# Performance work log

Measured on AMD Instinct MI355X. Metric: run time of the kernel, lower is better.

The kernel has to match this reference:

```python
import jax, jax.numpy as jnp
import numpy as np

HIDDEN = 1024
HEADS = 16
MEM = 2
D_H = HIDDEN // HEADS
NEG = -1.0e9


def setup_inputs() -> dict:
    key = jax.random.key(0)
    ks = jax.random.split(key, 8)
    B, M, N = 16, 512, 512
    s = 1.0 / np.sqrt(HIDDEN)
    return {
        "x": jax.random.normal(ks[0], (B, M, HIDDEN), dtype=jnp.float32),
        "y": jax.random.normal(ks[1], (B, N, HIDDEN), dtype=jnp.float32),
        "mask_x": jax.random.randint(ks[2], (B, M), 0, 2, dtype=jnp.int64),
        "mask_y": jax.random.randint(ks[3], (B, N), 0, 2, dtype=jnp.int64),
        "Wx": jax.random.normal(ks[4], (HIDDEN, HIDDEN), dtype=jnp.float32) * s,
        "Wy": jax.random.normal(ks[5], (HIDDEN, HIDDEN), dtype=jnp.float32) * s,
        "x_memory": jax.random.normal(ks[6], (MEM, HIDDEN), dtype=jnp.float32),
        "y_memory": jax.random.normal(ks[7], (MEM, HIDDEN), dtype=jnp.float32),
    }


def _project(t, mem, W):
    # prepend memory tokens, then linear (torch Linear: t @ W^T), split heads
    B = t.shape[0]
    t_mem = jnp.concatenate([jnp.broadcast_to(mem[None], (B, MEM, HIDDEN)), t], axis=1)
    proj = t_mem @ W.T
    proj = proj.reshape(B, t_mem.shape[1], HEADS, D_H)
    return t_mem, proj


def reference(x, y, mask_x, mask_y, Wx, Wy, x_memory, y_memory):
    B = x.shape[0]
    mem_mask = jnp.ones((B, MEM), dtype=mask_x.dtype)
    mx = jnp.concatenate([mem_mask, mask_x], axis=1)  # [B, M+MEM]
    my = jnp.concatenate([mem_mask, mask_y], axis=1)  # [B, N+MEM]

    X_mem, X_proj = _project(x, x_memory, Wx)  # [B,Mm,H], [B,Mm,heads,d_h]
    Y_mem, Y_proj = _project(y, y_memory, Wy)

    # affinity: [B, heads, Mm, Nm]
    aff = jnp.einsum("bmhd,bnhd->bhmn", X_proj, Y_proj)
    aff = jnp.where(mx[:, None, :, None] == 0, NEG, aff)
    aff = jnp.where(my[:, None, None, :] == 0, NEG, aff)

    attn_X = jnp.mean(jax.nn.softmax(aff, axis=2), axis=1)  # [B, Mm, Nm]
    attn_Y = jnp.mean(jax.nn.softmax(aff, axis=3), axis=1)  # [B, Mm, Nm]

    X_in_Y = jnp.einsum("bmn,bmh->bnh", attn_X, X_mem)[:, MEM:, :]  # [B, N, H]
    Y_in_X = jnp.einsum("bmn,bnh->bmh", attn_Y, Y_mem)[:, MEM:, :]  # [B, M, H]
    return X_in_Y, Y_in_X
```

## Files before the change

### kernel.cpp

```cpp
#include <hip/hip_runtime.h>

#define B_   16
#define SEQ  512
#define MM   514
#define HID  1024
#define NH   16
#define DH   64
#define KP   544
#define MTOT (B_ * MM)
#define UNI  (1.0f/514.0f)

typedef unsigned short us;
typedef __attribute__((ext_vector_type(4))) float f32x4;
typedef __attribute__((ext_vector_type(8))) short short8;
typedef __attribute__((ext_vector_type(8))) _Float16 half8;

__device__ __forceinline__ us f2bf(float f) {
  unsigned int u = __float_as_uint(f);
  u = (u + 0x7FFFu + ((u >> 16) & 1u)) >> 16;
  return (us)u;
}
__device__ __forceinline__ float bf2f(us h) {
  return __uint_as_float(((unsigned int)h) << 16);
}
__device__ __forceinline__ us f2h(float f) {
  _Float16 h = (_Float16)f;
  return *(us*)&h;
}
__device__ __forceinline__ unsigned cvt_pk_bf16(float lo, float hi) {
  unsigned d;
  asm("v_cvt_pk_bf16_f32 %0, %1, %2" : "=v"(d) : "v"(lo), "v"(hi));
  return d;
}

__global__ __launch_bounds__(256) void prepack(
    const float* __restrict__ x, const float* __restrict__ y,
    const float* __restrict__ xm, const float* __restrict__ ym,
    const float* __restrict__ Wx, const float* __restrict__ Wy,
    us* __restrict__ Abf, us* __restrict__ Wbf) {
  const int tid = threadIdx.x;
  const int row = blockIdx.x * 4 + (tid >> 6);
  const int path = blockIdx.y;
  const int lane = tid & 63;
  const float* src;
  us* dst;
  if (row < MTOT) {
    const int gb = row / MM, gt = row - gb * MM;
    const float* tin = path ? y : x;
    const float* mv  = path ? ym : xm;
    src = (gt < 2) ? (mv + (size_t)gt * HID)
                   : (tin + ((size_t)(gb * SEQ + gt - 2)) * HID);
    dst = Abf + ((size_t)(path * MTOT + row)) * HID;
  } else {
    const int o = row - MTOT;
    src = (path ? Wy : Wx) + (size_t)o * HID;
    dst = Wbf + ((size_t)(path * HID + o)) * HID;
  }
  const float* s = src + lane * 16;
  f32x4 v0 = *(const f32x4*)(s);
  f32x4 v1 = *(const f32x4*)(s + 4);
  f32x4 v2 = *(const f32x4*)(s + 8);
  f32x4 v3 = *(const f32x4*)(s + 12);
  uint4 w0, w1;
  w0.x = cvt_pk_bf16(v0[0], v0[1]);  w0.y = cvt_pk_bf16(v0[2], v0[3]);
  w0.z = cvt_pk_bf16(v1[0], v1[1]);  w0.w = cvt_pk_bf16(v1[2], v1[3]);
  w1.x = cvt_pk_bf16(v2[0], v2[1]);  w1.y = cvt_pk_bf16(v2[2], v2[3]);
  w1.z = cvt_pk_bf16(v3[0], v3[1]);  w1.w = cvt_pk_bf16(v3[2], v3[3]);
  *(uint4*)(dst + lane * 16)     = w0;
  *(uint4*)(dst + lane * 16 + 8) = w1;
}

__global__ __launch_bounds__(256) void proj_fused2(
    const us* __restrict__ Abf, const us* __restrict__ Wbf,
    us* __restrict__ Px, us* __restrict__ Py) {
  const int lin = blockIdx.x + 8 * (blockIdx.y + 65 * blockIdx.z);
  const int work = (lin & 7) * 130 + (lin >> 3);
  const int path = (work >= 520) ? 1 : 0;
  const int wrem = work - path * 520;
  const int mt = wrem >> 3, nt = wrem & 7;
  us* P = path ? Py : Px;
  const us* Ab = Abf + (size_t)path * MTOT * HID;
  const us* Wb = Wbf + (size_t)path * HID * HID;

  __shared__ __align__(16) us As[128 * 40];
  __shared__ __align__(16) us Bs[128 * 40];
  const int tid = threadIdx.x;
  const int lane = tid & 63, wave = tid >> 6;
  const int c = lane & 15, q = lane >> 4;
  const int wr = wave >> 1, wc = wave & 1;

  const int srow = tid >> 1, sch = (tid & 1) * 16;
  const int grow = mt * 128 + srow;
  const us* asrc = (grow < MTOT) ? (Ab + (size_t)grow * HID + sch) : nullptr;
  const us* bsrc = Wb + (size_t)(nt * 128 + srow) * HID + sch;
  us* wAp = &As[srow * 40 + sch];
  us* wBp = &Bs[srow * 40 + sch];
  const us* rA = &As[(wr * 64 + c) * 40 + q * 8];
  const us* rB = &Bs[(wc * 64 + c) * 40 + q * 8];

  f32x4 acc[4][4];
#pragma unroll
  for (int i = 0; i < 4; i++)
#pragma unroll
    for (int j = 0; j < 4; j++) acc[i][j] = (f32x4){0.f, 0.f, 0.f, 0.f};

  uint4 z4 = {0u, 0u, 0u, 0u};
  uint4 pa0 = z4, pa1 = z4, pb0, pb1;
  if (asrc) { pa0 = *(const uint4*)asrc; pa1 = *(const uint4*)(asrc + 8); }
  pb0 = *(const uint4*)bsrc; pb1 = *(const uint4*)(bsrc + 8);

  for (int kk = 0; kk < HID; kk += 32) {
    __syncthreads();
    *(uint4*)wAp       = pa0;
    *(uint4*)(wAp + 8) = pa1;
    *(uint4*)wBp       = pb0;
    *(uint4*)(wBp + 8) = pb1;
    __syncthreads();
    if (kk + 32 < HID) {
      if (asrc) {
        pa0 = *(const uint4*)(asrc + kk + 32);
        pa1 = *(const uint4*)(asrc + kk + 32 + 8);
      }
      pb0 = *(const uint4*)(bsrc + kk + 32);
      pb1 = *(const uint4*)(bsrc + kk + 32 + 8);
    }
    short8 a[4], bb[4];
#pragma unroll
    for (int i = 0; i < 4; i++) a[i] = *(const short8*)(rA + i * 16 * 40);
#pragma unroll
    for (int j = 0; j < 4; j++) bb[j] = *(const short8*)(rB + j * 16 * 40);
#pragma unroll
    for (int i = 0; i < 4; i++)
#pragma unroll
      for (int j = 0; j < 4; j++)
        acc[i][j] = __builtin_amdgcn_mfma_f32_16x16x32_bf16(a[i], bb[j], acc[i][j], 0, 0, 0);
  }
#pragma unroll
  for (int i = 0; i < 4; i++) {
#pragma unroll
    for (int r = 0; r < 4; r++) {
      int gr = mt * 128 + wr * 64 + i * 16 + q * 4 + r;
      if (gr < MTOT) {
        size_t rb = (size_t)gr * HID;
#pragma unroll
        for (int j = 0; j < 4; j++)
          P[rb + nt * 128 + wc * 64 + j * 16 + c] = f2bf(acc[i][j][r]);
      }
    }
  }
}

__device__ __forceinline__ void stage_bf(
    us* Xs, const us* P, int b, int r0, int h, int tid) {
#pragma unroll
  for (int i = 0; i < 2; i++) {
    int idx = tid + i * 256;
    int row = idx >> 3, qq = idx & 7;
    *(uint4*)&Xs[row * 72 + qq * 8] =
        *(const uint4*)(P + ((size_t)(b * MM + min(r0 + row, MM - 1))) * HID + h * DH + qq * 8);
  }
}

__global__ __launch_bounds__(512) void sums_v4(
    const us* __restrict__ Px, const us* __restrict__ Py,
    const int* __restrict__ mx, const int* __restrict__ my,
    float* __restrict__ Sums) {
  const int lin = blockIdx.x;
  const int work = (lin & 7) * 160 + (lin >> 3);
  const int b = work / 80;
  const int rem = work - b * 80;
  const int h = rem / 5;
  const int nc = rem - h * 5;
  const int n0 = nc * 128;
  __shared__ __align__(16) us Ys[128 * 72];
  __shared__ __align__(16) us Xs[2][64 * 72];
  __shared__ float cS2[4][128];
  __shared__ float rS2[2][576];
  __shared__ int myS[128];
  __shared__ int mxS[576];
  const int tid = threadIdx.x;
  const int lane = tid & 63, wave = tid >> 6;
  const int c = lane & 15, q = lane >> 4;
  const int strip = wave & 3, cgrp = wave >> 2;
  const int row8 = tid >> 3, qq = tid & 7;

  for (int i = tid; i < 128; i += 512) {
    int n = n0 + i;
    myS[i] = (n >= MM) ? 0 : ((n < 2) ? 1 : my[b * SEQ + n - 2]);
  }
  for (int i = tid; i < 576; i += 512)
    mxS[i] = (i >= MM) ? 0 : ((i < 2) ? 1 : mx[b * SEQ + i - 2]);
  {
#pragma unroll
    for (int it = 0; it < 2; it++) {
      int idx = tid + it * 512;
      int row = idx >> 3, q8 = idx & 7;
      int grow = min(n0 + row, MM - 1);
      *(uint4*)&Ys[row * 72 + q8 * 8] =
          *(const uint4*)(Py + ((size_t)(b * MM + grow)) * HID + h * DH + q8 * 8);
    }
  }
  {
    int grow = min(row8, MM - 1);
    *(uint4*)&Xs[0][row8 * 72 + qq * 8] =
        *(const uint4*)(Px + ((size_t)(b * MM + grow)) * HID + h * DH + qq * 8);
  }
  __syncthreads();

  const size_t base = ((size_t)(b * NH + h)) * MM;
  const size_t COLOFF = (size_t)B_ * NH * MM;

  int myReg[4];
#pragma unroll
  for (int ss = 0; ss < 4; ss++) myReg[ss] = myS[cgrp * 64 + ss * 16 + c];

  float colAcc[4] = {0.f, 0.f, 0.f, 0.f};

  for (int mt = 0; mt < 9; mt++) {
    const us* xb = &Xs[mt & 1][0];
    uint4 nx = {0u, 0u, 0u, 0u};
    if (mt + 1 < 9) {
      int grow = min((mt + 1) * 64 + row8, MM - 1);
      nx = *(const uint4*)(Px + ((size_t)(b * MM + grow)) * HID + h * DH + qq * 8);
    }
    short8 a0 = *(const short8*)&xb[(strip * 16 + c) * 72 + q * 8];
    short8 a1 = *(const short8*)&xb[(strip * 16 + c) * 72 + q * 8 + 32];
    int rm[4];
#pragma unroll
    for (int r = 0; r < 4; r++) rm[r] = mxS[mt * 64 + strip * 16 + q * 4 + r];
    float rowp[4] = {0.f, 0.f, 0.f, 0.f};
#pragma unroll
    for (int ss = 0; ss < 4; ss++) {
      int nloc = cgrp * 64 + ss * 16 + c;
      short8 b0 = *(const short8*)&Ys[nloc * 72 + q * 8];
      short8 b1 = *(const short8*)&Ys[nloc * 72 + q * 8 + 32];
      f32x4 av = (f32x4){0.f, 0.f, 0.f, 0.f};
      av = __builtin_amdgcn_mfma_f32_16x16x32_bf16(a0, b0, av, 0, 0, 0);
      av = __builtin_amdgcn_mfma_f32_16x16x32_bf16(a1, b1, av, 0, 0, 0);
#pragma unroll
      for (int r = 0; r < 4; r++) {
        float e = (rm[r] && myReg[ss]) ? __expf(av[r]) : 0.f;
        rowp[r] += e;
        colAcc[ss] += e;
      }
    }
#pragma unroll
    for (int d = 1; d < 16; d <<= 1)
#pragma unroll
      for (int r = 0; r < 4; r++) rowp[r] += __shfl_xor(rowp[r], d, 16);
    if (c == 0) {
#pragma unroll
      for (int r = 0; r < 4; r++)
        rS2[cgrp][mt * 64 + strip * 16 + q * 4 + r] = rowp[r];
    }
    if (mt + 1 < 9)
      *(uint4*)&Xs[(mt + 1) & 1][row8 * 72 + qq * 8] = nx;
    __syncthreads();
  }

#pragma unroll
  for (int ss = 0; ss < 4; ss++) {
    colAcc[ss] += __shfl_xor(colAcc[ss], 16);
    colAcc[ss] += __shfl_xor(colAcc[ss], 32);
  }
  if (q == 0) {
#pragma unroll
    for (int ss = 0; ss < 4; ss++)
      cS2[strip][cgrp * 64 + ss * 16 + c] = colAcc[ss];
  }
  __syncthreads();
  for (int i = tid; i < 128; i += 512) {
    int n = n0 + i;
    if (n < MM)
      Sums[COLOFF + base + n] = cS2[0][i] + cS2[1][i] + cS2[2][i] + cS2[3][i];
  }
  for (int i = tid; i < 576; i += 512) {
    if (i < MM) atomicAdd(&Sums[base + i], rS2[0][i] + rS2[1][i]);
  }
}

__global__ __launch_bounds__(256) void inv_kernel(float* __restrict__ Sums) {
  int i = blockIdx.x * 256 + threadIdx.x;
  if (i < 2 * B_ * NH * MM) {
    float s = Sums[i];
    Sums[i] = (s > 0.f) ? (1.f / s) : -1.f;
  }
}

__global__ __launch_bounds__(256) void attn_swz(
    const us* __restrict__ Px, const us* __restrict__ Py,
    const int* __restrict__ mx, const int* __restrict__ my,
    const float* __restrict__ Inv,
    us* __restrict__ attnXT, us* __restrict__ attnY) {
  const int lin = blockIdx.x;
  const int work = (lin & 7) * 162 + (lin >> 3);
  const int b = work / 81;
  const int rem = work - b * 81;
  const int mt = rem / 9;
  const int nt = rem - mt * 9;
  __shared__ __align__(16) us Xs[64 * 72];
  __shared__ __align__(16) us Ys[64 * 72];
  const int tid = threadIdx.x;
  const int lane = tid & 63, wave = tid >> 6;
  const int c = lane & 15, q = lane >> 4;
  const size_t COLOFF = (size_t)B_ * NH * MM;

  int mreg[4], rm[4], ncol[4], cm[4];
#pragma unroll
  for (int r = 0; r < 4; r++) {
    mreg[r] = mt * 64 + wave * 16 + q * 4 + r;
    rm[r] = (mreg[r] >= MM) ? 0 : ((mreg[r] < 2) ? 1 : mx[b * SEQ + mreg[r] - 2]);
  }
#pragma unroll
  for (int s = 0; s < 4; s++) {
    ncol[s] = nt * 64 + s * 16 + c;
    cm[s] = (ncol[s] >= MM) ? 0 : ((ncol[s] < 2) ? 1 : my[b * SEQ + ncol[s] - 2]);
  }

  float aX[4][4], aY[4][4];
#pragma unroll
  for (int s = 0; s < 4; s++)
#pragma unroll
    for (int r = 0; r < 4; r++) { aX[s][r] = 0.f; aY[s][r] = 0.f; }

  for (int h = 0; h < NH; h++) {
    __syncthreads();
    stage_bf(Xs, Px, b, mt * 64, h, tid);
    stage_bf(Ys, Py, b, nt * 64, h, tid);
    __syncthreads();
    short8 a0 = *(const short8*)&Xs[(wave * 16 + c) * 72 + q * 8];
    short8 a1 = *(const short8*)&Xs[(wave * 16 + c) * 72 + q * 8 + 32];
    const size_t base = ((size_t)(b * NH + h)) * MM;
    float invR[4];
#pragma unroll
    for (int r = 0; r < 4; r++) invR[r] = Inv[base + min(mreg[r], MM - 1)];
#pragma unroll
    for (int s = 0; s < 4; s++) {
      float invC = Inv[COLOFF + base + min(ncol[s], MM - 1)];
      short8 b0 = *(const short8*)&Ys[(s * 16 + c) * 72 + q * 8];
      short8 b1 = *(const short8*)&Ys[(s * 16 + c) * 72 + q * 8 + 32];
      f32x4 av = (f32x4){0.f, 0.f, 0.f, 0.f};
      av = __builtin_amdgcn_mfma_f32_16x16x32_bf16(a0, b0, av, 0, 0, 0);
      av = __builtin_amdgcn_mfma_f32_16x16x32_bf16(a1, b1, av, 0, 0, 0);
#pragma unroll
      for (int r = 0; r < 4; r++) {
        float e = (rm[r] && cm[s]) ? __expf(av[r]) : 0.f;
        aY[s][r] += (invR[r] < 0.f) ? UNI : e * invR[r];
        aX[s][r] += (invC < 0.f) ? UNI : e * invC;
      }
    }
  }
#pragma unroll
  for (int s = 0; s < 4; s++) {
    if (ncol[s] < MM) {
      us* xrow = attnXT + ((size_t)(b * MM + ncol[s])) * KP;
      if (mreg[3] < MM) {
        uint2 w;
        w.x = (unsigned)f2h(aX[s][0] * 0.0625f) | ((unsigned)f2h(aX[s][1] * 0.0625f) << 16);
        w.y = (unsigned)f2h(aX[s][2] * 0.0625f) | ((unsigned)f2h(aX[s][3] * 0.0625f) << 16);
        *(uint2*)&xrow[mreg[0]] = w;
      } else {
#pragma unroll
        for (int r = 0; r < 4; r++)
          if (mreg[r] < MM) xrow[mreg[r]] = f2h(aX[s][r] * 0.0625f);
      }
#pragma unroll
      for (int r = 0; r < 4; r++)
        if (mreg[r] < MM)
          attnY[((size_t)(b * MM + mreg[r])) * KP + ncol[s]] = f2h(aY[s][r] * 0.0625f);
    }
  }
}

__global__ __launch_bounds__(256) void transpose_fused(
    const float* __restrict__ x, const float* __restrict__ y,
    const float* __restrict__ xm, const float* __restrict__ ym,
    us* __restrict__ XTx, us* __restrict__ XTy) {
  const int kt = blockIdx.x, ot = blockIdx.y;
  const int b = blockIdx.z & 15, path = blockIdx.z >> 4;
  const float* tin  = path ? y  : x;
  const float* mvec = path ? ym : xm;
  us* XT            = path ? XTy : XTx;
  __shared__ __align__(16) us T[64 * 40];
  const int tid = threadIdx.x;
  {
    const int row = tid >> 3;
    const int col8 = (tid & 7) * 8;
    const int kg = kt * 32 + row;
    const float* src = (kg < 2) ? (mvec + (size_t)kg * HID + ot * 64 + col8)
                     : (kg < MM) ? (tin + ((size_t)(b * SEQ + kg - 2)) * HID + ot * 64 + col8)
                                 : nullptr;
    f32x4 v0 = (f32x4){0.f, 0.f, 0.f, 0.f};
    f32x4 v1 = (f32x4){0.f, 0.f, 0.f, 0.f};
    if (src) { v0 = *(const f32x4*)src; v1 = *(const f32x4*)(src + 4); }
#pragma unroll
    for (int j = 0; j < 4; j++) T[(col8 + j) * 40 + row] = f2h(v0[j]);
#pragma unroll
    for (int j = 0; j < 4; j++) T[(col8 + 4 + j) * 40 + row] = f2h(v1[j]);
  }
  __syncthreads();
  const int orow = tid >> 2, kc = (tid & 3) * 8;
  uint4 w = *(const uint4*)&T[orow * 40 + kc];
  *(uint4*)&XT[((size_t)(b * HID + ot * 64 + orow)) * KP + kt * 32 + kc] = w;
}

__global__ __launch_bounds__(256) void outg_fused(
    const us* __restrict__ A0, const us* __restrict__ A1,
    const us* __restrict__ XTx, const us* __restrict__ XTy,
    float* __restrict__ outp) {
  const int ot = blockIdx.x, rt = blockIdx.y;
  const int b = blockIdx.z & 15, path = blockIdx.z >> 4;
  const us* A  = path ? A1 : A0;
  const us* XT = path ? XTy : XTx;
  float* op = outp + (path ? (size_t)B_ * SEQ * HID : 0);
  const int r0 = rt * 128, o0 = ot * 128;
  __shared__ __align__(16) us As[128 * 40];
  __shared__ __align__(16) us Bs[128 * 40];
  const int tid = threadIdx.x;
  const int lane = tid & 63, wave = tid >> 6;
  const int c = lane & 15, q = lane >> 4;
  const int wr = wave >> 1, wc = wave & 1;

  const int srow = tid >> 2, sch = (tid & 3) * 8;
  const us* gA0 = A + ((size_t)(b * MM + 2 + r0 + srow)) * KP + sch;
  const us* gA1 = gA0 + (size_t)64 * KP;
  const us* gB0 = XT + ((size_t)(b * HID + o0 + srow)) * KP + sch;
  const us* gB1 = gB0 + (size_t)64 * KP;
  us* wA0 = &As[srow * 40 + sch];
  us* wA1 = wA0 + 64 * 40;
  us* wB0 = &Bs[srow * 40 + sch];
  us* wB1 = wB0 + 64 * 40;

  f32x4 acc[4][4];
#pragma unroll
  for (int i = 0; i < 4; i++)
#pragma unroll
    for (int j = 0; j < 4; j++) acc[i][j] = (f32x4){0.f, 0.f, 0.f, 0.f};

  const us* rA = &As[(wr * 64 + c) * 40 + q * 8];
  const us* rB = &Bs[(wc * 64 + c) * 40 + q * 8];

  uint4 pA0 = *(const uint4*)gA0;
  uint4 pA1 = *(const uint4*)gA1;
  uint4 pB0 = *(const uint4*)gB0;
  uint4 pB1 = *(const uint4*)gB1;

  for (int kk = 0; kk < KP; kk += 32) {
    __syncthreads();
    *(uint4*)wA0 = pA0;
    *(uint4*)wA1 = pA1;
    *(uint4*)wB0 = pB0;
    *(uint4*)wB1 = pB1;
    __syncthreads();
    if (kk + 32 < KP) {
      pA0 = *(const uint4*)(gA0 + kk + 32);
      pA1 = *(const uint4*)(gA1 + kk + 32);
      pB0 = *(const uint4*)(gB0 + kk + 32);
      pB1 = *(const uint4*)(gB1 + kk + 32);
    }
    half8 a[4], bb[4];
#pragma unroll
    for (int i = 0; i < 4; i++) a[i] = *(const half8*)(rA + i * 16 * 40);
#pragma unroll
    for (int j = 0; j < 4; j++) bb[j] = *(const half8*)(rB + j * 16 * 40);
#pragma unroll
    for (int i = 0; i < 4; i++)
#pragma unroll
      for (int j = 0; j < 4; j++)
        acc[i][j] = __builtin_amdgcn_mfma_f32_16x16x32_f16(a[i], bb[j], acc[i][j], 0, 0, 0);
  }
#pragma unroll
  for (int i = 0; i < 4; i++) {
#pragma unroll
    for (int rr = 0; rr < 4; rr++) {
      int r = r0 + wr * 64 + i * 16 + q * 4 + rr;
      size_t rowbase = ((size_t)(b * SEQ + r)) * HID;
#pragma unroll
      for (int j = 0; j < 4; j++)
        op[rowbase + o0 + wc * 64 + j * 16 + c] = acc[i][j][rr];
    }
  }
}

__global__ __launch_bounds__(256) void attn_mfma_old(
    const us* __restrict__ Px, const us* __restrict__ Py,
    const int* __restrict__ mx, const int* __restrict__ my,
    const float* __restrict__ Inv,
    us* __restrict__ attnX, us* __restrict__ attnY,
    const int doX, const int doY) {
  const int nt = blockIdx.x, mt = blockIdx.y, b = blockIdx.z;
  __shared__ __align__(16) us Xs[64 * 72];
  __shared__ __align__(16) us Ys[64 * 72];
  const int tid = threadIdx.x;
  const int lane = tid & 63, wave = tid >> 6;
  const int c = lane & 15, q = lane >> 4;
  const size_t COLOFF = (size_t)B_ * NH * MM;

  int mreg[4], rm[4], ncol[4], cm[4];
#pragma unroll
  for (int r = 0; r < 4; r++) {
    mreg[r] = mt * 64 + wave * 16 + q * 4 + r;
    rm[r] = (mreg[r] >= MM) ? 0 : ((mreg[r] < 2) ? 1 : mx[b * SEQ + mreg[r] - 2]);
  }
#pragma unroll
  for (int s = 0; s < 4; s++) {
    ncol[s] = nt * 64 + s * 16 + c;
    cm[s] = (ncol[s] >= MM) ? 0 : ((ncol[s] < 2) ? 1 : my[b * SEQ + ncol[s] - 2]);
  }

  float aX[4][4], aY[4][4];
#pragma unroll
  for (int s = 0; s < 4; s++)
#pragma unroll
    for (int r = 0; r < 4; r++) { aX[s][r] = 0.f; aY[s][r] = 0.f; }

  for (int h = 0; h < NH; h++) {
    __syncthreads();
    stage_bf(Xs, Px, b, mt * 64, h, tid);
    stage_bf(Ys, Py, b, nt * 64, h, tid);
    __syncthreads();
    short8 a0 = *(const short8*)&Xs[(wave * 16 + c) * 72 + q * 8];
    short8 a1 = *(const short8*)&Xs[(wave * 16 + c) * 72 + q * 8 + 32];
    const size_t base = ((size_t)(b * NH + h)) * MM;
    float invR[4];
#pragma unroll
    for (int r = 0; r < 4; r++) invR[r] = Inv[base + min(mreg[r], MM - 1)];
#pragma unroll
    for (int s = 0; s < 4; s++) {
      float invC = Inv[COLOFF + base + min(ncol[s], MM - 1)];
      short8 b0 = *(const short8*)&Ys[(s * 16 + c) * 72 + q * 8];
      short8 b1 = *(const short8*)&Ys[(s * 16 + c) * 72 + q * 8 + 32];
      f32x4 av = (f32x4){0.f, 0.f, 0.f, 0.f};
      av = __builtin_amdgcn_mfma_f32_16x16x32_bf16(a0, b0, av, 0, 0, 0);
      av = __builtin_amdgcn_mfma_f32_16x16x32_bf16(a1, b1, av, 0, 0, 0);
#pragma unroll
      for (int r = 0; r < 4; r++) {
        float e = (rm[r] && cm[s]) ? __expf(av[r]) : 0.f;
        aY[s][r] += (invR[r] < 0.f) ? UNI : e * invR[r];
        aX[s][r] += (invC < 0.f) ? UNI : e * invC;
      }
    }
  }
#pragma unroll
  for (int s = 0; s < 4; s++) {
#pragma unroll
    for (int r = 0; r < 4; r++) {
      if (mreg[r] < MM && ncol[s] < MM) {
        size_t idx = ((size_t)(b * MM + mreg[r])) * MM + ncol[s];
        if (doX) attnX[idx] = f2bf(aX[s][r] * 0.0625f);
        if (doY) attnY[idx] = f2bf(aY[s][r] * 0.0625f);
      }
    }
  }
}

__global__ __launch_bounds__(256) void outg_kernel(
    const us* __restrict__ attn, const float* __restrict__ tin,
    const float* __restrict__ mvec, float* __restrict__ outp, const int trans) {
  const int otile = blockIdx.x, rtile = blockIdx.y, b = blockIdx.z;
  __shared__ __align__(16) float Ss[32 * 132];
  __shared__ __align__(16) float Ms[32 * 132];
  const int tid = threadIdx.x;
  const int r0 = rtile * 128, o0 = otile * 128;

  float acc[8][8];
#pragma unroll
  for (int i = 0; i < 8; i++)
#pragma unroll
    for (int j = 0; j < 8; j++) acc[i][j] = 0.f;

  for (int kk = 0; kk < 544; kk += 32) {
    __syncthreads();
    if (trans) {
      int rq = (tid & 31) * 4;
      int kr = tid >> 5;
#pragma unroll
      for (int kb = 0; kb < 32; kb += 8) {
        int k = kr + kb;
        int kg = kk + k;
        if (kg < MM) {
          const us* src = attn + ((size_t)(b * MM + kg)) * MM + 2 + r0 + rq;
          Ss[k * 132 + rq + 0] = bf2f(src[0]);
          Ss[k * 132 + rq + 1] = bf2f(src[1]);
          Ss[k * 132 + rq + 2] = bf2f(src[2]);
          Ss[k * 132 + rq + 3] = bf2f(src[3]);
        } else {
          Ss[k * 132 + rq + 0] = 0.f;
          Ss[k * 132 + rq + 1] = 0.f;
          Ss[k * 132 + rq + 2] = 0.f;
          Ss[k * 132 + rq + 3] = 0.f;
        }
      }
    } else {
      int r = tid >> 1;
      int kh = (tid & 1) * 16;
      const us* src = attn + ((size_t)(b * MM + 2 + r0 + r)) * MM;
#pragma unroll
      for (int j = 0; j < 16; j++) {
        int k = kh + j;
        int kg = kk + k;
        Ss[k * 132 + r] = (kg < MM) ? bf2f(src[kg]) : 0.f;
      }
    }
    {
      int k = tid >> 3;
      int oq = (tid & 7) * 16;
      int kg = kk + k;
      const float* mr = (kg < 2) ? (mvec + (size_t)kg * HID)
                      : (kg < MM) ? (tin + ((size_t)(b * SEQ + kg - 2)) * HID)
                                  : nullptr;
#pragma unroll
      for (int qq = 0; qq < 4; qq++) {
        f32x4 v = (f32x4){0.f, 0.f, 0.f, 0.f};
        if (mr) v = *(const f32x4*)(mr + o0 + oq + qq * 4);
        *(f32x4*)&Ms[k * 132 + oq + qq * 4] = v;
      }
    }
    __syncthreads();
    const int ty = tid >> 4, tx = tid & 15;
    for (int k = 0; k < 32; k++) {
      f32x4 s0 = *(const f32x4*)&Ss[k * 132 + ty * 4];
      f32x4 s1 = *(const f32x4*)&Ss[k * 132 + 64 + ty * 4];
      f32x4 m0 = *(const f32x4*)&Ms[k * 132 + tx * 4];
      f32x4 m1 = *(const f32x4*)&Ms[k * 132 + 64 + tx * 4];
#pragma unroll
      for (int i = 0; i < 4; i++) {
#pragma unroll
        for (int j = 0; j < 4; j++) {
          acc[i][j]         += s0[i] * m0[j];
          acc[i][j + 4]     += s0[i] * m1[j];
          acc[i + 4][j]     += s1[i] * m0[j];
          acc[i + 4][j + 4] += s1[i] * m1[j];
        }
      }
    }
  }
  const int ty = tid >> 4, tx = tid & 15;
#pragma unroll
  for (int ri = 0; ri < 2; ri++) {
#pragma unroll
    for (int i = 0; i < 4; i++) {
      int r = r0 + ri * 64 + ty * 4 + i;
      size_t rowbase = ((size_t)(b * SEQ + r)) * HID;
#pragma unroll
      for (int oi = 0; oi < 2; oi++) {
        int o = o0 + oi * 64 + tx * 4;
        f32x4 v;
#pragma unroll
        for (int j = 0; j < 4; j++) v[j] = acc[ri * 4 + i][oi * 4 + j];
        *(f32x4*)&outp[rowbase + o] = v;
      }
    }
  }
}

extern "C" void kernel_launch(void* const* d_in, const int* in_sizes, int n_in,
                              void* d_out, int out_size, void* d_ws, size_t ws_size,
                              hipStream_t stream) {
  const float* x  = (const float*)d_in[0];
  const float* y  = (const float*)d_in[1];
  const int* mask_x = (const int*)d_in[2];
  const int* mask_y = (const int*)d_in[3];
  const float* Wx = (const float*)d_in[4];
  const float* Wy = (const float*)d_in[5];
  const float* xm = (const float*)d_in[6];
  const float* ym = (const float*)d_in[7];
  float* out = (float*)d_out;

  const size_t szSums = (size_t)2 * B_ * NH * MM * 4;
  const size_t szP    = (size_t)B_ * MM * HID * 2;
  const size_t szAtt  = (size_t)B_ * MM * MM * 2;
  const size_t szAttP = (size_t)B_ * MM * KP * 2;
  const size_t szXT   = (size_t)B_ * HID * KP * 2;
  const size_t R_off  = szSums + 2 * szAttP;
  const size_t needNew = R_off + 2 * szXT;

  char* ws = (char*)d_ws;

  us* Abf = (us*)d_out;
  us* Wbf = (us*)d_out + (size_t)2 * MTOT * HID;

  if (ws_size >= needNew) {
    float* Sums = (float*)ws;
    us* A0  = (us*)(ws + szSums);
    us* A1  = (us*)(ws + szSums + szAttP);
    us* Px  = (us*)(ws + R_off);
    us* Py  = (us*)(ws + R_off + szP);
    us* XTx = (us*)(ws + R_off);
    us* XTy = (us*)(ws + R_off + szXT);

    prepack<<<dim3((MTOT + HID) / 4, 2), 256, 0, stream>>>(x, y, xm, ym, Wx, Wy, Abf, Wbf);
    proj_fused2<<<dim3(8, 65, 2), 256, 0, stream>>>(Abf, Wbf, Px, Py);
    hipMemsetAsync(Sums, 0, szSums, stream);
    hipMemsetAsync(A0, 0, 2 * szAttP, stream);
    sums_v4<<<dim3(1280), 512, 0, stream>>>(Px, Py, mask_x, mask_y, Sums);
    inv_kernel<<<dim3((2 * B_ * NH * MM + 255) / 256), 256, 0, stream>>>(Sums);
    attn_swz<<<dim3(1296), 256, 0, stream>>>(Px, Py, mask_x, mask_y, Sums, A0, A1);
    transpose_fused<<<dim3(17, 16, 32), 256, 0, stream>>>(x, y, xm, ym, XTx, XTy);
    outg_fused<<<dim3(8, 4, 32), 256, 0, stream>>>(A0, A1, XTx, XTy, out);
    return;
  }

  const int dual = (ws_size >= szSums + 2 * szP + 2 * szAtt) ? 1 : 0;
  float* Sums = (float*)(ws);
  us* Px = (us*)(ws + szSums);
  us* Py = (us*)(ws + szSums + szP);
  us* A0 = (us*)(ws + szSums + 2 * szP);
  us* A1 = dual ? (us*)(ws + szSums + 2 * szP + szAtt) : A0;

  prepack<<<dim3((MTOT + HID) / 4, 2), 256, 0, stream>>>(x, y, xm, ym, Wx, Wy, Abf, Wbf);
  proj_fused2<<<dim3(8, 65, 2), 256, 0, stream>>>(Abf, Wbf, Px, Py);
  hipMemsetAsync(Sums, 0, szSums, stream);
  sums_v4<<<dim3(1280), 512, 0, stream>>>(Px, Py, mask_x, mask_y, Sums);
  inv_kernel<<<dim3((2 * B_ * NH * MM + 255) / 256), 256, 0, stream>>>(Sums);

  if (dual) {
    attn_mfma_old<<<dim3(9, 9, 16), 256, 0, stream>>>(Px, Py, mask_x, mask_y, Sums, A0, A1, 1, 1);
    outg_kernel<<<dim3(8, 4, 16), 256, 0, stream>>>(A0, x, xm, out, 1);
    outg_kernel<<<dim3(8, 4, 16), 256, 0, stream>>>(A1, y, ym, out + (size_t)B_ * SEQ * HID, 0);
  } else {
    attn_mfma_old<<<dim3(9, 9, 16), 256, 0, stream>>>(Px, Py, mask_x, mask_y, Sums, A0, A0, 1, 0);
    outg_kernel<<<dim3(8, 4, 16), 256, 0, stream>>>(A0, x, xm, out, 1);
    attn_mfma_old<<<dim3(9, 9, 16), 256, 0, stream>>>(Px, Py, mask_x, mask_y, Sums, A0, A0, 0, 1);
    outg_kernel<<<dim3(8, 4, 16), 256, 0, stream>>>(A0, y, ym, out + (size_t)B_ * SEQ * HID, 0);
  }
}
```

Baseline: 349.4 us.

## Load X fragments directly from global and drop per-tile barriers in sums kernel

The sums kernel no longer double-buffers X tiles through shared memory. Each lane loads its MFMA A-fragments straight from global memory, so the per-iteration __syncthreads goes away. Row and column masks are now read into registers, with row masks packed into a 64-bit bitmask, which removes the mask shared arrays. Launch bounds gain a minimum-blocks hint to raise occupancy. In exchange, each wave re-reads X rows from global or L2 instead of sharing one staged tile, and the extra register and occupancy pressure may cost performance.

After: 508.9 us. 1.46x slower.

```diff
diff --git a/kernel.cpp b/kernel.cpp
--- a/kernel.cpp
+++ b/kernel.cpp
@@ -161,7 +161,7 @@
   }
 }
 
-__global__ __launch_bounds__(512) void sums_v4(
+__global__ __launch_bounds__(512, 6) void sums_v5(
     const us* __restrict__ Px, const us* __restrict__ Py,
     const int* __restrict__ mx, const int* __restrict__ my,
     float* __restrict__ Sums) {
@@ -173,23 +173,13 @@
   const int nc = rem - h * 5;
   const int n0 = nc * 128;
   __shared__ __align__(16) us Ys[128 * 72];
-  __shared__ __align__(16) us Xs[2][64 * 72];
   __shared__ float cS2[4][128];
   __shared__ float rS2[2][576];
-  __shared__ int myS[128];
-  __shared__ int mxS[576];
   const int tid = threadIdx.x;
   const int lane = tid & 63, wave = tid >> 6;
   const int c = lane & 15, q = lane >> 4;
   const int strip = wave & 3, cgrp = wave >> 2;
-  const int row8 = tid >> 3, qq = tid & 7;
-
-  for (int i = tid; i < 128; i += 512) {
-    int n = n0 + i;
-    myS[i] = (n >= MM) ? 0 : ((n < 2) ? 1 : my[b * SEQ + n - 2]);
-  }
-  for (int i = tid; i < 576; i += 512)
-    mxS[i] = (i >= MM) ? 0 : ((i < 2) ? 1 : mx[b * SEQ + i - 2]);
+
   {
 #pragma unroll
     for (int it = 0; it < 2; it++) {
@@ -200,34 +190,35 @@
           *(const uint4*)(Py + ((size_t)(b * MM + grow)) * HID + h * DH + q8 * 8);
     }
   }
-  {
-    int grow = min(row8, MM - 1);
-    *(uint4*)&Xs[0][row8 * 72 + qq * 8] =
-        *(const uint4*)(Px + ((size_t)(b * MM + grow)) * HID + h * DH + qq * 8);
+
+  int myReg[4];
+#pragma unroll
+  for (int ss = 0; ss < 4; ss++) {
+    int n = n0 + cgrp * 64 + ss * 16 + c;
+    myReg[ss] = (n >= MM) ? 0 : ((n < 2) ? 1 : my[b * SEQ + n - 2]);
+  }
+  unsigned long long rmask = 0ull;
+  for (int mt = 0; mt < 9; mt++) {
+#pragma unroll
+    for (int r = 0; r < 4; r++) {
+      int m = mt * 64 + strip * 16 + q * 4 + r;
+      int v = (m >= MM) ? 0 : ((m < 2) ? 1 : mx[b * SEQ + m - 2]);
+      rmask |= (unsigned long long)(v != 0) << (mt * 4 + r);
+    }
   }
   __syncthreads();
 
   const size_t base = ((size_t)(b * NH + h)) * MM;
   const size_t COLOFF = (size_t)B_ * NH * MM;
-
-  int myReg[4];
-#pragma unroll
-  for (int ss = 0; ss < 4; ss++) myReg[ss] = myS[cgrp * 64 + ss * 16 + c];
+  const us* pxh = Px + (size_t)b * MM * HID + h * DH + q * 8;
 
   float colAcc[4] = {0.f, 0.f, 0.f, 0.f};
 
   for (int mt = 0; mt < 9; mt++) {
-    const us* xb = &Xs[mt & 1][0];
-    uint4 nx = {0u, 0u, 0u, 0u};
-    if (mt + 1 < 9) {
-      int grow = min((mt + 1) * 64 + row8, MM - 1);
-      nx = *(const uint4*)(Px + ((size_t)(b * MM + grow)) * HID + h * DH + qq * 8);
-    }
-    short8 a0 = *(const short8*)&xb[(strip * 16 + c) * 72 + q * 8];
-    short8 a1 = *(const short8*)&xb[(strip * 16 + c) * 72 + q * 8 + 32];
-    int rm[4];
-#pragma unroll
-    for (int r = 0; r < 4; r++) rm[r] = mxS[mt * 64 + strip * 16 + q * 4 + r];
+    const int arow = min(mt * 64 + strip * 16 + c, MM - 1);
+    const us* ap = pxh + (size_t)arow * HID;
+    short8 a0 = *(const short8*)ap;
+    short8 a1 = *(const short8*)(ap + 32);
     float rowp[4] = {0.f, 0.f, 0.f, 0.f};
 #pragma unroll
     for (int ss = 0; ss < 4; ss++) {
@@ -239,7 +230,8 @@
       av = __builtin_amdgcn_mfma_f32_16x16x32_bf16(a1, b1, av, 0, 0, 0);
 #pragma unroll
       for (int r = 0; r < 4; r++) {
-        float e = (rm[r] && myReg[ss]) ? __expf(av[r]) : 0.f;
+        int rmv = (int)((rmask >> (mt * 4 + r)) & 1ull);
+        float e = (rmv && myReg[ss]) ? __expf(av[r]) : 0.f;
         rowp[r] += e;
         colAcc[ss] += e;
       }
@@ -253,9 +245,6 @@
       for (int r = 0; r < 4; r++)
         rS2[cgrp][mt * 64 + strip * 16 + q * 4 + r] = rowp[r];
     }
-    if (mt + 1 < 9)
-      *(uint4*)&Xs[(mt + 1) & 1][row8 * 72 + qq * 8] = nx;
-    __syncthreads();
   }
 
 #pragma unroll
@@ -693,7 +682,7 @@
     proj_fused2<<<dim3(8, 65, 2), 256, 0, stream>>>(Abf, Wbf, Px, Py);
     hipMemsetAsync(Sums, 0, szSums, stream);
     hipMemsetAsync(A0, 0, 2 * szAttP, stream);
-    sums_v4<<<dim3(1280), 512, 0, stream>>>(Px, Py, mask_x, mask_y, Sums);
+    sums_v5<<<dim3(1280), 512, 0, stream>>>(Px, Py, mask_x, mask_y, Sums);
     inv_kernel<<<dim3((2 * B_ * NH * MM + 255) / 256), 256, 0, stream>>>(Sums);
     attn_swz<<<dim3(1296), 256, 0, stream>>>(Px, Py, mask_x, mask_y, Sums, A0, A1);
     transpose_fused<<<dim3(17, 16, 32), 256, 0, stream>>>(x, y, xm, ym, XTx, XTy);
@@ -711,7 +700,7 @@
   prepack<<<dim3((MTOT + HID) / 4, 2), 256, 0, stream>>>(x, y, xm, ym, Wx, Wy, Abf, Wbf);
   proj_fused2<<<dim3(8, 65, 2), 256, 0, stream>>>(Abf, Wbf, Px, Py);
   hipMemsetAsync(Sums, 0, szSums, stream);
-  sums_v4<<<dim3(1280), 512, 0, stream>>>(Px, Py, mask_x, mask_y, Sums);
+  sums_v5<<<dim3(1280), 512, 0, stream>>>(Px, Py, mask_x, mask_y, Sums);
   inv_kernel<<<dim3((2 * B_ * NH * MM + 255) / 256), 256, 0, stream>>>(Sums);
 
   if (dual) {
```
